# Kernel optimization log

Hardware: AMD Instinct MI355X
Metric: run time of the kernel (lower is better)

## Reference

```python
import jax, jax.numpy as jnp
import numpy as np

N = 50000      # nodes
E = 800000     # edges (avg degree 16)
D_IN = 64
D_H = 64
D_OUT = 64


def setup_inputs() -> dict:
    key = jax.random.key(0)
    ks = jax.random.split(key, 8)
    x = jax.random.normal(ks[0], (N, D_IN), dtype=jnp.float32)
    edge_index = jax.random.randint(ks[1], (2, E), 0, N, dtype=jnp.int32)
    s1 = 1.0 / np.sqrt(D_IN)
    s2 = 1.0 / np.sqrt(D_H)
    s3 = 1.0 / np.sqrt(D_OUT)
    W1 = jax.random.uniform(ks[2], (D_IN, D_H), jnp.float32, -s1, s1)
    b1 = jnp.zeros((D_H,), jnp.float32)
    W2 = jax.random.uniform(ks[3], (D_H, D_OUT), jnp.float32, -s2, s2)
    b2 = jnp.zeros((D_OUT,), jnp.float32)
    Wfc = jax.random.uniform(ks[4], (D_OUT, 1), jnp.float32, -s3, s3)
    bfc = jax.random.uniform(ks[5], (1,), jnp.float32, -s3, s3)
    return {"x": x, "edge_index": edge_index, "W1": W1, "b1": b1,
            "W2": W2, "b2": b2, "Wfc": Wfc, "bfc": bfc}


def gcn_conv(x, W, b, src, dst, norm, n):
    """PyG GCNConv: h = x@W; out_i = sum_{(s,i)} norm * h_s ; + bias."""
    h = x @ W                                     # [N, d_out]
    msg = h[src] * norm[:, None]                  # [E+N, d_out] gather
    agg = jax.ops.segment_sum(msg, dst, num_segments=n)  # scatter-add
    return agg + b


def reference(x, edge_index, W1, b1, W2, b2, Wfc, bfc):
    n = x.shape[0]
    # add self-loops (PyG default add_self_loops=True)
    loops = jnp.arange(n, dtype=edge_index.dtype)
    src = jnp.concatenate([edge_index[0], loops])
    dst = jnp.concatenate([edge_index[1], loops])
    # symmetric normalization deg^{-1/2} (deg computed with self-loops, >=1)
    deg = jnp.zeros((n,), x.dtype).at[dst].add(1.0)
    dinv = jax.lax.rsqrt(deg)
    norm = dinv[src] * dinv[dst]                  # [E+N]
    h = jax.nn.relu(gcn_conv(x, W1, b1, src, dst, norm, n))
    # dropout is identity in eval mode
    h = jax.nn.relu(gcn_conv(h, W2, b2, src, dst, norm, n))
    out = h @ Wfc + bfc                           # [N, 1]
    out = jnp.mean(out, axis=0, keepdims=True)    # [1, 1]
    return jax.nn.sigmoid(out)
```

## Files before the change

kernel.cpp:

```cpp
#include <hip/hip_runtime.h>
#include <hip/hip_fp16.h>
#include <math.h>

#define N_NODES 50000
#define N_EDGES 800000
#define D_FEAT 64

#define NBUCKET 196
#define PART_BLOCKS 391
#define PART_EPB 2048
#define BCAP 6144

#define GEMM_BLOCKS (N_NODES / 16)
#define AGG_UNITS 1568
#define N_PAD (NBUCKET * 256)

typedef float v2f __attribute__((ext_vector_type(2)));


__device__ __forceinline__ unsigned pack_fp8x4(float a, float b, float c, float d) {
    unsigned w = 0;
    w = __builtin_amdgcn_cvt_pk_fp8_f32(a, b, w, false);
    w = __builtin_amdgcn_cvt_pk_fp8_f32(c, d, w, true);
    return w;
}

__device__ __forceinline__ void addf8(float acc[8], uint2 r) {
    v2f f0 = __builtin_amdgcn_cvt_pk_f32_fp8(r.x, false);
    v2f f1 = __builtin_amdgcn_cvt_pk_f32_fp8(r.x, true);
    v2f f2 = __builtin_amdgcn_cvt_pk_f32_fp8(r.y, false);
    v2f f3 = __builtin_amdgcn_cvt_pk_f32_fp8(r.y, true);
    acc[0] += f0[0]; acc[1] += f0[1];
    acc[2] += f1[0]; acc[3] += f1[1];
    acc[4] += f2[0]; acc[5] += f2[1];
    acc[6] += f3[0]; acc[7] += f3[1];
}


__global__ __launch_bounds__(256) void k_zero(int* __restrict__ gcount) {
    if (threadIdx.x < NBUCKET) gcount[threadIdx.x] = 0;
}

__global__ __launch_bounds__(256) void k_part(const int* __restrict__ src,
                                              const int* __restrict__ dst,
                                              int* __restrict__ gcount,
                                              unsigned* __restrict__ ebuf) {
    __shared__ int cnt[NBUCKET];
    int tid = threadIdx.x;
    for (int i = tid; i < NBUCKET; i += 256) cnt[i] = 0;
    __syncthreads();
    int e0 = blockIdx.x * PART_EPB;
    unsigned pw[8];
    #pragma unroll
    for (int u = 0; u < 8; ++u) {
        int e = e0 + u * 256 + tid;
        pw[u] = 0xFFFFFFFFu;
        if (e < N_EDGES) {
            int d = dst[e];
            pw[u] = (unsigned)src[e] | ((unsigned)(d & 255) << 16) | ((unsigned)(d >> 8) << 24);
            atomicAdd(&cnt[d >> 8], 1);
        }
    }
    __syncthreads();
    for (int i = tid; i < NBUCKET; i += 256)
        cnt[i] = atomicAdd(&gcount[i], cnt[i]);
    __syncthreads();
    #pragma unroll
    for (int u = 0; u < 8; ++u) {
        unsigned p = pw[u];
        int b = p >> 24;
        if (b < NBUCKET) {
            int slot = atomicAdd(&cnt[b], 1);
            if (slot < BCAP) ebuf[(size_t)b * BCAP + slot] = p;
        }
    }
}

__global__ __launch_bounds__(512) void k_p2group(const unsigned* __restrict__ ebuf,
                                                 const int* __restrict__ gcount,
                                                 int* __restrict__ rowbeg,
                                                 int* __restrict__ rowdeg,
                                                 ushort* __restrict__ colsrc,
                                                 float* __restrict__ dinv) {
    __shared__ unsigned eloc[BCAP];
    __shared__ int hist[256];
    __shared__ int sh[256];
    int tid = threadIdx.x;
    int b = blockIdx.x;
    int cnt = gcount[b]; if (cnt > BCAP) cnt = BCAP;
    if (tid < 256) hist[tid] = 0;
    __syncthreads();
    for (int i = tid; i < cnt; i += 512) {
        unsigned p = ebuf[(size_t)b * BCAP + i];
        eloc[i] = p;
        atomicAdd(&hist[(p >> 16) & 255], 1);
    }
    __syncthreads();
    int v = (tid < 256) ? hist[tid] : 0;
    if (tid < 256) sh[tid] = v;
    __syncthreads();
    #pragma unroll
    for (int off = 1; off < 256; off <<= 1) {
        int t = (tid >= off && tid < 256) ? sh[tid - off] : 0;
        __syncthreads();
        if (tid < 256) sh[tid] += t;
        __syncthreads();
    }
    if (tid < 256) {
        int binoff = sh[tid] - v;
        int node = b * 256 + tid;
        rowbeg[node] = b * BCAP + binoff;
        rowdeg[node] = v;
        dinv[node] = rsqrtf((float)(v + 1));
        hist[tid] = binoff;
    }
    __syncthreads();
    for (int i = tid; i < cnt; i += 512) {
        unsigned p = eloc[i];
        int slot = b * BCAP + atomicAdd(&hist[(p >> 16) & 255], 1);
        colsrc[slot] = (ushort)(p & 0xFFFFu);
    }
}


__global__ __launch_bounds__(256) void k_gemm_f32(const float* __restrict__ X,
                                                  const float* __restrict__ W,
                                                  const float* __restrict__ dinv,
                                                  unsigned* __restrict__ out8) {
    __shared__ float Wl[64][64];
    int tid = threadIdx.x;
    {
        const float4* Wv = (const float4*)W;
        float4* Wlv = (float4*)&Wl[0][0];
        #pragma unroll
        for (int i = 0; i < 4; ++i) Wlv[tid + 256 * i] = Wv[tid + 256 * i];
    }
    __syncthreads();
    int r = blockIdx.x * 16 + (tid >> 4);
    int c0 = (tid & 15) << 2;
    const float4* xrow = (const float4*)(X + (size_t)r * D_FEAT);
    float ax = 0.f, ay = 0.f, az = 0.f, aw = 0.f;
    #pragma unroll
    for (int k4 = 0; k4 < 16; ++k4) {
        float4 xv = xrow[k4];
        #pragma unroll
        for (int j = 0; j < 4; ++j) {
            float xs = (j == 0) ? xv.x : (j == 1) ? xv.y : (j == 2) ? xv.z : xv.w;
            const float4 wv = *(const float4*)&Wl[4 * k4 + j][c0];
            ax += xs * wv.x; ay += xs * wv.y; az += xs * wv.z; aw += xs * wv.w;
        }
    }
    float sc = dinv[r];
    out8[r * 16 + (c0 >> 2)] = pack_fp8x4(ax * sc, ay * sc, az * sc, aw * sc);
}


__device__ __forceinline__ void agg_core(const unsigned char* __restrict__ hm,
                                         const ushort* __restrict__ colsrc,
                                         int beg, int deg, int o, float acc[8]) {
    const uint2* hv = (const uint2*)hm;
    int j = 0;
    for (; j + 16 <= deg; j += 16) {
        int s[16]; uint2 r[16];
        #pragma unroll
        for (int u = 0; u < 16; ++u) s[u] = colsrc[beg + j + u];
        #pragma unroll
        for (int u = 0; u < 16; ++u) r[u] = hv[(size_t)s[u] * 8 + o];
        #pragma unroll
        for (int u = 0; u < 16; ++u) addf8(acc, r[u]);
    }
    if (j + 8 <= deg) {
        int s[8]; uint2 r[8];
        #pragma unroll
        for (int u = 0; u < 8; ++u) s[u] = colsrc[beg + j + u];
        #pragma unroll
        for (int u = 0; u < 8; ++u) r[u] = hv[(size_t)s[u] * 8 + o];
        #pragma unroll
        for (int u = 0; u < 8; ++u) addf8(acc, r[u]);
        j += 8;
    }
    if (j + 4 <= deg) {
        int s[4]; uint2 r[4];
        #pragma unroll
        for (int u = 0; u < 4; ++u) s[u] = colsrc[beg + j + u];
        #pragma unroll
        for (int u = 0; u < 4; ++u) r[u] = hv[(size_t)s[u] * 8 + o];
        #pragma unroll
        for (int u = 0; u < 4; ++u) addf8(acc, r[u]);
        j += 4;
    }
    for (; j < deg; ++j) {
        int s = colsrc[beg + j];
        addf8(acc, hv[(size_t)s * 8 + o]);
    }
}


__global__ __launch_bounds__(256) void k_agg1_g2(const unsigned char* __restrict__ hm,
                                                 const int* __restrict__ rowbeg,
                                                 const int* __restrict__ rowdeg,
                                                 const ushort* __restrict__ colsrc,
                                                 const float* __restrict__ dinv,
                                                 const float* __restrict__ b1,
                                                 const float* __restrict__ W2,
                                                 unsigned char* __restrict__ outp) {
    __shared__ float Wl[64][64];
    {
        const float4* Wv = (const float4*)W2;
        float4* Wlv = (float4*)&Wl[0][0];
        #pragma unroll
        for (int i = 0; i < 4; ++i) Wlv[threadIdx.x + 256 * i] = Wv[threadIdx.x + 256 * i];
    }
    __syncthreads();
    int lane = threadIdx.x & 63;
    int wid = threadIdx.x >> 6;
    int node = (blockIdx.x * 4 + wid) * 8 + (lane >> 3);
    int o = lane & 7;
    if (node < N_NODES) {
        float acc[8];
        #pragma unroll
        for (int i = 0; i < 8; ++i) acc[i] = 0.f;
        const uint2* hv = (const uint2*)hm;
        addf8(acc, hv[(size_t)node * 8 + o]);
        agg_core(hm, colsrc, rowbeg[node], rowdeg[node], o, acc);
        float di = dinv[node];
        const float4* b4 = (const float4*)b1;
        float4 bl = b4[o * 2], bh = b4[o * 2 + 1];
        float h1[8];
        h1[0] = fmaxf(di * acc[0] + bl.x, 0.f);
        h1[1] = fmaxf(di * acc[1] + bl.y, 0.f);
        h1[2] = fmaxf(di * acc[2] + bl.z, 0.f);
        h1[3] = fmaxf(di * acc[3] + bl.w, 0.f);
        h1[4] = fmaxf(di * acc[4] + bh.x, 0.f);
        h1[5] = fmaxf(di * acc[5] + bh.y, 0.f);
        h1[6] = fmaxf(di * acc[6] + bh.z, 0.f);
        h1[7] = fmaxf(di * acc[7] + bh.w, 0.f);
        float oa[8];
        #pragma unroll
        for (int i = 0; i < 8; ++i) oa[i] = 0.f;
        int gbase = lane & 56;
        #pragma unroll
        for (int g = 0; g < 8; ++g) {
            #pragma unroll
            for (int j = 0; j < 8; ++j) {
                float hk = __shfl(h1[j], gbase | g, 64);
                const float4 w0 = *(const float4*)&Wl[g * 8 + j][o * 8];
                const float4 w1 = *(const float4*)&Wl[g * 8 + j][o * 8 + 4];
                oa[0] += hk * w0.x; oa[1] += hk * w0.y;
                oa[2] += hk * w0.z; oa[3] += hk * w0.w;
                oa[4] += hk * w1.x; oa[5] += hk * w1.y;
                oa[6] += hk * w1.z; oa[7] += hk * w1.w;
            }
        }
        uint2 st;
        st.x = pack_fp8x4(oa[0] * di, oa[1] * di, oa[2] * di, oa[3] * di);
        st.y = pack_fp8x4(oa[4] * di, oa[5] * di, oa[6] * di, oa[7] * di);
        *(uint2*)(outp + (size_t)node * D_FEAT + o * 8) = st;
    }
}


__global__ __launch_bounds__(256) void k_agg2_dot(const unsigned char* __restrict__ hm,
                                                  const int* __restrict__ rowbeg,
                                                  const int* __restrict__ rowdeg,
                                                  const ushort* __restrict__ colsrc,
                                                  const float* __restrict__ dinv,
                                                  const float* __restrict__ bias,
                                                  const float* __restrict__ Wfc,
                                                  float* __restrict__ partials) {
    __shared__ float red[4];
    int lane = threadIdx.x & 63;
    int wid = threadIdx.x >> 6;
    int node = (blockIdx.x * 4 + wid) * 8 + (lane >> 3);
    int o = lane & 7;
    float s = 0.f;
    if (node < N_NODES) {
        float acc[8];
        #pragma unroll
        for (int i = 0; i < 8; ++i) acc[i] = 0.f;
        const uint2* hv = (const uint2*)hm;
        addf8(acc, hv[(size_t)node * 8 + o]);
        agg_core(hm, colsrc, rowbeg[node], rowdeg[node], o, acc);
        float di = dinv[node];
        const float4* b4 = (const float4*)bias;
        const float4* w4 = (const float4*)Wfc;
        float4 bl = b4[o * 2], bh = b4[o * 2 + 1];
        float4 wl = w4[o * 2], wh = w4[o * 2 + 1];
        s  = fmaxf(di * acc[0] + bl.x, 0.f) * wl.x;
        s += fmaxf(di * acc[1] + bl.y, 0.f) * wl.y;
        s += fmaxf(di * acc[2] + bl.z, 0.f) * wl.z;
        s += fmaxf(di * acc[3] + bl.w, 0.f) * wl.w;
        s += fmaxf(di * acc[4] + bh.x, 0.f) * wh.x;
        s += fmaxf(di * acc[5] + bh.y, 0.f) * wh.y;
        s += fmaxf(di * acc[6] + bh.z, 0.f) * wh.z;
        s += fmaxf(di * acc[7] + bh.w, 0.f) * wh.w;
    }
    #pragma unroll
    for (int m = 1; m < 64; m <<= 1) s += __shfl_xor(s, m, 64);
    if (lane == 0) red[wid] = s;
    __syncthreads();
    if (threadIdx.x == 0) partials[blockIdx.x] = red[0] + red[1] + red[2] + red[3];
}

__global__ __launch_bounds__(256) void k_final(const float* __restrict__ partials,
                                               const float* __restrict__ bfc,
                                               float* __restrict__ out) {
    __shared__ float red[4];
    float s = 0.0f;
    for (int i = threadIdx.x; i < AGG_UNITS; i += 256) s += partials[i];
    #pragma unroll
    for (int off = 32; off > 0; off >>= 1) s += __shfl_down(s, off, 64);
    if ((threadIdx.x & 63) == 0) red[threadIdx.x >> 6] = s;
    __syncthreads();
    if (threadIdx.x == 0) {
        float t = red[0] + red[1] + red[2] + red[3];
        float z = t / (float)N_NODES + bfc[0];
        out[0] = 1.0f / (1.0f + expf(-z));
    }
}


extern "C" void kernel_launch(void* const* d_in, const int* in_sizes, int n_in,
                              void* d_out, int out_size, void* d_ws, size_t ws_size,
                              hipStream_t stream) {
    const float* x   = (const float*)d_in[0];
    const int*   ei  = (const int*)d_in[1];
    const int*   src = ei;
    const int*   dst = ei + N_EDGES;
    const float* W1  = (const float*)d_in[2];
    const float* b1  = (const float*)d_in[3];
    const float* W2  = (const float*)d_in[4];
    const float* b2  = (const float*)d_in[5];
    const float* Wfc = (const float*)d_in[6];
    const float* bfc = (const float*)d_in[7];
    float* out = (float*)d_out;

    char* ws = (char*)d_ws;
    size_t off = 0;
    auto alloc = [&](size_t bytes) -> char* {
        char* p = ws + off;
        off += (bytes + 255) & ~(size_t)255;
        return p;
    };
    int*           gcount   = (int*)alloc((size_t)NBUCKET * 4);
    unsigned*      ebuf     = (unsigned*)alloc((size_t)NBUCKET * BCAP * 4);
    ushort*        colsrc   = (ushort*)alloc((size_t)NBUCKET * BCAP * 2);
    int*           rowbeg   = (int*)alloc((size_t)N_PAD * 4);
    int*           rowdeg   = (int*)alloc((size_t)N_PAD * 4);
    float*         dinv     = (float*)alloc((size_t)N_PAD * 4);
    float*         partials = (float*)alloc((size_t)AGG_UNITS * 4);
    unsigned char* bufA     = (unsigned char*)alloc((size_t)N_NODES * D_FEAT);
    unsigned char* bufB     = (unsigned char*)alloc((size_t)N_NODES * D_FEAT);

    k_zero     <<<1,           256, 0, stream>>>(gcount);
    k_part     <<<PART_BLOCKS, 256, 0, stream>>>(src, dst, gcount, ebuf);
    k_p2group  <<<NBUCKET,     512, 0, stream>>>(ebuf, gcount, rowbeg, rowdeg, colsrc, dinv);

    k_gemm_f32 <<<GEMM_BLOCKS, 256, 0, stream>>>(x, W1, dinv, (unsigned*)bufA);

    k_agg1_g2  <<<AGG_UNITS,   256, 0, stream>>>(bufA, rowbeg, rowdeg, colsrc, dinv, b1, W2, bufB);

    k_agg2_dot <<<AGG_UNITS,   256, 0, stream>>>(bufB, rowbeg, rowdeg, colsrc, dinv, b2, Wfc, partials);

    k_final    <<<1,           256, 0, stream>>>(partials, bfc, out);
}
```

Measured before the change: 83.65 us.

## Sort nodes by degree within buckets to balance aggregation wavefronts

The grouping kernel now builds a per-bucket permutation that orders each bucket's 256 nodes by in-degree, capped at 63, using a shared histogram and prefix sum. Both aggregation kernels read node ids through this permutation. The aim is to put nodes of similar degree in the same wavefront so lanes stop idling while they wait for the highest-degree node. The gather loop's main unroll drops from 16 to 8, and the zeroing kernel is replaced by hipMemsetAsync. The cost is an extra indirection load, less contiguous output writes, slightly more work in the grouping kernel, and less memory-level parallelism per loop iteration.

```diff
diff --git a/kernel.cpp b/kernel.cpp
--- a/kernel.cpp
+++ b/kernel.cpp
@@ -37,10 +37,6 @@
 }
 
 
-__global__ __launch_bounds__(256) void k_zero(int* __restrict__ gcount) {
-    if (threadIdx.x < NBUCKET) gcount[threadIdx.x] = 0;
-}
-
 __global__ __launch_bounds__(256) void k_part(const int* __restrict__ src,
                                               const int* __restrict__ dst,
                                               int* __restrict__ gcount,
@@ -81,14 +77,17 @@
                                                  int* __restrict__ rowbeg,
                                                  int* __restrict__ rowdeg,
                                                  ushort* __restrict__ colsrc,
-                                                 float* __restrict__ dinv) {
+                                                 float* __restrict__ dinv,
+                                                 int* __restrict__ order) {
     __shared__ unsigned eloc[BCAP];
     __shared__ int hist[256];
     __shared__ int sh[256];
+    __shared__ int bin2[64];
     int tid = threadIdx.x;
     int b = blockIdx.x;
     int cnt = gcount[b]; if (cnt > BCAP) cnt = BCAP;
     if (tid < 256) hist[tid] = 0;
+    if (tid >= 256 && tid < 320) bin2[tid - 256] = 0;
     __syncthreads();
     for (int i = tid; i < cnt; i += 512) {
         unsigned p = ebuf[(size_t)b * BCAP + i];
@@ -106,6 +105,7 @@
         if (tid < 256) sh[tid] += t;
         __syncthreads();
     }
+    int bin = (v < 63) ? v : 63;
     if (tid < 256) {
         int binoff = sh[tid] - v;
         int node = b * 256 + tid;
@@ -113,6 +113,18 @@
         rowdeg[node] = v;
         dinv[node] = rsqrtf((float)(v + 1));
         hist[tid] = binoff;
+        atomicAdd(&bin2[bin], 1);
+    }
+    __syncthreads();
+    if (tid == 0) {
+        int run = 0;
+        #pragma unroll
+        for (int i = 0; i < 64; ++i) { int c = bin2[i]; bin2[i] = run; run += c; }
+    }
+    __syncthreads();
+    if (tid < 256) {
+        int r = atomicAdd(&bin2[bin], 1);
+        order[b * 256 + r] = b * 256 + tid;
     }
     __syncthreads();
     for (int i = tid; i < cnt; i += 512) {
@@ -160,16 +172,7 @@
                                          int beg, int deg, int o, float acc[8]) {
     const uint2* hv = (const uint2*)hm;
     int j = 0;
-    for (; j + 16 <= deg; j += 16) {
-        int s[16]; uint2 r[16];
-        #pragma unroll
-        for (int u = 0; u < 16; ++u) s[u] = colsrc[beg + j + u];
-        #pragma unroll
-        for (int u = 0; u < 16; ++u) r[u] = hv[(size_t)s[u] * 8 + o];
-        #pragma unroll
-        for (int u = 0; u < 16; ++u) addf8(acc, r[u]);
-    }
-    if (j + 8 <= deg) {
+    for (; j + 8 <= deg; j += 8) {
         int s[8]; uint2 r[8];
         #pragma unroll
         for (int u = 0; u < 8; ++u) s[u] = colsrc[beg + j + u];
@@ -177,7 +180,6 @@
         for (int u = 0; u < 8; ++u) r[u] = hv[(size_t)s[u] * 8 + o];
         #pragma unroll
         for (int u = 0; u < 8; ++u) addf8(acc, r[u]);
-        j += 8;
     }
     if (j + 4 <= deg) {
         int s[4]; uint2 r[4];
@@ -201,6 +203,7 @@
                                                  const int* __restrict__ rowdeg,
                                                  const ushort* __restrict__ colsrc,
                                                  const float* __restrict__ dinv,
+                                                 const int* __restrict__ order,
                                                  const float* __restrict__ b1,
                                                  const float* __restrict__ W2,
                                                  unsigned char* __restrict__ outp) {
@@ -214,7 +217,7 @@
     __syncthreads();
     int lane = threadIdx.x & 63;
     int wid = threadIdx.x >> 6;
-    int node = (blockIdx.x * 4 + wid) * 8 + (lane >> 3);
+    int node = order[(blockIdx.x * 4 + wid) * 8 + (lane >> 3)];
     int o = lane & 7;
     if (node < N_NODES) {
         float acc[8];
@@ -265,13 +268,14 @@
                                                   const int* __restrict__ rowdeg,
                                                   const ushort* __restrict__ colsrc,
                                                   const float* __restrict__ dinv,
+                                                  const int* __restrict__ order,
                                                   const float* __restrict__ bias,
                                                   const float* __restrict__ Wfc,
                                                   float* __restrict__ partials) {
     __shared__ float red[4];
     int lane = threadIdx.x & 63;
     int wid = threadIdx.x >> 6;
-    int node = (blockIdx.x * 4 + wid) * 8 + (lane >> 3);
+    int node = order[(blockIdx.x * 4 + wid) * 8 + (lane >> 3)];
     int o = lane & 7;
     float s = 0.f;
     if (node < N_NODES) {
@@ -348,19 +352,20 @@
     int*           rowbeg   = (int*)alloc((size_t)N_PAD * 4);
     int*           rowdeg   = (int*)alloc((size_t)N_PAD * 4);
     float*         dinv     = (float*)alloc((size_t)N_PAD * 4);
+    int*           order    = (int*)alloc((size_t)N_PAD * 4);
     float*         partials = (float*)alloc((size_t)AGG_UNITS * 4);
     unsigned char* bufA     = (unsigned char*)alloc((size_t)N_NODES * D_FEAT);
     unsigned char* bufB     = (unsigned char*)alloc((size_t)N_NODES * D_FEAT);
 
-    k_zero     <<<1,           256, 0, stream>>>(gcount);
+    hipMemsetAsync(gcount, 0, (size_t)NBUCKET * 4, stream);
     k_part     <<<PART_BLOCKS, 256, 0, stream>>>(src, dst, gcount, ebuf);
-    k_p2group  <<<NBUCKET,     512, 0, stream>>>(ebuf, gcount, rowbeg, rowdeg, colsrc, dinv);
+    k_p2group  <<<NBUCKET,     512, 0, stream>>>(ebuf, gcount, rowbeg, rowdeg, colsrc, dinv, order);
 
     k_gemm_f32 <<<GEMM_BLOCKS, 256, 0, stream>>>(x, W1, dinv, (unsigned*)bufA);
 
-    k_agg1_g2  <<<AGG_UNITS,   256, 0, stream>>>(bufA, rowbeg, rowdeg, colsrc, dinv, b1, W2, bufB);
-
-    k_agg2_dot <<<AGG_UNITS,   256, 0, stream>>>(bufB, rowbeg, rowdeg, colsrc, dinv, b2, Wfc, partials);
+    k_agg1_g2  <<<AGG_UNITS,   256, 0, stream>>>(bufA, rowbeg, rowdeg, colsrc, dinv, order, b1, W2, bufB);
+
+    k_agg2_dot <<<AGG_UNITS,   256, 0, stream>>>(bufB, rowbeg, rowdeg, colsrc, dinv, order, b2, Wfc, partials);
 
     k_final    <<<1,           256, 0, stream>>>(partials, bfc, out);
 }
```

Result: no change. 84.78 us (+1.3%).
